# Kernel optimization log

Hardware: AMD Instinct MI355X
Metric: run time of the kernel (lower is better)

The kernel has to match this reference:

```python
import jax, jax.numpy as jnp
import numpy as np

PH, PW, RANK, N_ITER = 7, 7, 8, 5


def _khatri_rao(a, b):
    # a:[I,R], b:[J,R] -> [I*J,R], row index i*J+j (tensorly convention)
    return (a[:, None, :] * b[None, :, :]).reshape(-1, a.shape[1])


def _unfold(t, mode):
    return jnp.moveaxis(t, mode, 0).reshape(t.shape[mode], -1)


def cp_als(t, rank, n_iter, key):
    # CP decomposition via ALS (tensorly parafac, init='random', fixed n_iter,
    # normalize_factors=False -> weights are ones)
    dims = t.shape
    keys = jax.random.split(key, len(dims))
    factors = [jax.random.uniform(keys[i], (dims[i], rank), dtype=t.dtype)
               for i in range(len(dims))]
    unfoldings = [_unfold(t, n) for n in range(len(dims))]
    for _ in range(n_iter):
        for n in range(len(dims)):
            others = [factors[m] for m in range(len(dims)) if m != n]
            kr = _khatri_rao(others[0], others[1])
            mttkrp = unfoldings[n] @ kr
            v = (others[0].T @ others[0]) * (others[1].T @ others[1])
            factors[n] = mttkrp @ jnp.linalg.pinv(v)
    return jnp.ones((rank,), dtype=t.dtype), factors


def setup_inputs() -> dict:
    key = jax.random.key(0)
    k1, _ = jax.random.split(key)
    x = jax.random.normal(k1, (8, 64, 224, 224), dtype=jnp.float32)
    beta = jnp.zeros((1,), dtype=jnp.float32)
    return {"x": x, "beta": beta}


def reference(x, beta):
    B, C, H, W = x.shape
    Hb, Wb = H // PH, W // PW
    M, P = Hb * Wb, PH * PW
    # unfold (kernel == stride, non-overlapping) -> FM:[B*M, P, C]
    FM = x.reshape(B, C, Hb, PH, Wb, PW).transpose(0, 2, 4, 3, 5, 1)
    FM = FM.reshape(B * M, P, C)
    # patch-wise attention scores [B*M, P, P]
    Sc = jax.nn.softmax(jnp.einsum('npc,nqc->npq', FM, FM), axis=-1)
    # patch-wise covariance (mean over channel dim)
    FMc = FM - FM.mean(axis=-1, keepdims=True)
    cov_big = jnp.einsum('npc,nqc->npq', FMc, FMc) / C
    cov_global = cov_big.mean(axis=0, keepdims=True)  # [1, P, P]
    # CP(ALS) decomposition of the global covariance tensor
    weights, (f0, f1, f2) = cp_als(cov_global, RANK, N_ITER, jax.random.key(42))
    w = weights * f0[0]                      # [rank]
    cov_cp = (f1 * w[None, :]) @ f2.T        # [P, P]
    L = Sc + cov_cp[None, :, :]
    Ec = jnp.einsum('npq,nqc->npc', L, FM)   # [B*M, P, C]
    # fold back to [B, C, H, W]
    Ec_map = Ec.reshape(B, Hb, Wb, PH, PW, C).transpose(0, 5, 1, 3, 2, 4)
    Ec_map = Ec_map.reshape(B, C, H, W)
    att_map = beta * Ec_map + x
    out = x * att_map
    return (out, Sc.reshape(B, M, P, P), cov_big.reshape(B, M, P, P), Ec_map)
```

## Files before the change

kernel.cpp:

```cpp
#include <hip/hip_runtime.h>

#define NPATCH   8192
#define PP2      2401
#define CH_STR   50176
#define B_STR    3211264
#define OFF_SC   25690112
#define OFF_COV  45359104
#define OFF_EC   65028096

__device__ __forceinline__ unsigned rotl32(unsigned v, unsigned r){ return (v<<r)|(v>>(32u-r)); }

__device__ __forceinline__ void threefry2x32(unsigned k0, unsigned k1,
                                             unsigned x0, unsigned x1,
                                             unsigned &o0, unsigned &o1){
  unsigned ks2 = k0 ^ k1 ^ 0x1BD11BDAu;
  x0 += k0; x1 += k1;
#define TFR(r) x0 += x1; x1 = rotl32(x1,(r)); x1 ^= x0;
  TFR(13) TFR(15) TFR(26) TFR(6)
  x0 += k1;  x1 += ks2 + 1u;
  TFR(17) TFR(29) TFR(16) TFR(24)
  x0 += ks2; x1 += k0 + 2u;
  TFR(13) TFR(15) TFR(26) TFR(6)
  x0 += k0;  x1 += k1 + 3u;
  TFR(17) TFR(29) TFR(16) TFR(24)
  x0 += k1;  x1 += ks2 + 4u;
  TFR(13) TFR(15) TFR(26) TFR(6)
  x0 += ks2; x1 += k0 + 5u;
#undef TFR
  o0 = x0; o1 = x1;
}

__device__ __forceinline__ float u01f(unsigned b){
  return __uint_as_float((b>>9) | 0x3f800000u) - 1.0f;
}

__global__ __launch_bounds__(256) void k_stats(const float* __restrict__ x,
                                               float* __restrict__ sc_out,
                                               float* __restrict__ cov_out){
  __shared__ float fmt[4][64*49];
  __shared__ float mbuf[4][49], mxb[4][49], ivb[4][49];
  const int t = threadIdx.x, w = t>>6, lane = t&63;
  const int n = (blockIdx.x<<2) + w;
  const int b = n>>10, rem = n&1023, hb = rem>>5, wb = rem&31;
  const float* xp = x + b*B_STR + (hb*7)*224 + wb*7;
  float* fm = fmt[w];

  for (int i=0;i<49;i++){
    int idx = lane + (i<<6);
    int c = idx/49; int p = idx - 49*c; int ph = p/7; int pw = p - 7*ph;
    fm[c*49+p] = xp[c*CH_STR + ph*224 + pw];
  }
  __syncthreads();

  if (lane < 49){
    float s = 0.f;
    for (int k=0;k<64;k++) s += fm[k*49+lane];
    mbuf[w][lane] = s * 0.015625f;
  }

  {
    const int ti = lane/7, tj = lane - 7*(lane/7);
    float acc[7][7];
    if (lane < 49){
      #pragma unroll
      for (int r=0;r<7;r++)
        #pragma unroll
        for (int s=0;s<7;s++) acc[r][s] = 0.f;
      for (int k=0;k<64;k++){
        float av[7], bv[7];
        #pragma unroll
        for (int r=0;r<7;r++) av[r] = fm[k*49 + 7*ti + r];
        #pragma unroll
        for (int s=0;s<7;s++) bv[s] = fm[k*49 + 7*tj + s];
        #pragma unroll
        for (int r=0;r<7;r++)
          #pragma unroll
          for (int s=0;s<7;s++) acc[r][s] = fmaf(av[r], bv[s], acc[r][s]);
      }
    }
    __syncthreads();
    if (lane < 49){
      #pragma unroll
      for (int r=0;r<7;r++)
        #pragma unroll
        for (int s=0;s<7;s++) fm[(7*ti+r)*49 + 7*tj + s] = acc[r][s];
    }
  }
  __syncthreads();

  if (lane < 49){
    float mx = -3.0e38f;
    for (int q=0;q<49;q++) mx = fmaxf(mx, fm[lane*49+q]);
    float s = 0.f;
    for (int q=0;q<49;q++) s += __expf(fm[lane*49+q]-mx);
    mxb[w][lane] = mx; ivb[w][lane] = 1.f/s;
  }
  __syncthreads();

  float* scp = sc_out + (long)n*PP2;
  float* cvp = cov_out + (long)n*PP2;
  for (int i=lane;i<PP2;i+=64){
    int p = i/49, q = i - 49*p;
    float g = fm[i];
    scp[i] = __expf(g - mxb[w][p]) * ivb[w][p];
    cvp[i] = g*0.015625f - mbuf[w][p]*mbuf[w][q];
  }
}

__global__ __launch_bounds__(256) void k_reduce(const float* __restrict__ cov,
                                                double* __restrict__ part){
  const int c = blockIdx.x;
  const float* base = cov + (long)c*32*PP2;
  for (int i=threadIdx.x; i<PP2; i+=256){
    double a0=0.0,a1=0.0,a2=0.0,a3=0.0;
    #pragma unroll
    for (int n=0;n<32;n+=4){
      a0 += (double)base[(n+0)*PP2+i];
      a1 += (double)base[(n+1)*PP2+i];
      a2 += (double)base[(n+2)*PP2+i];
      a3 += (double)base[(n+3)*PP2+i];
    }
    part[(long)c*PP2+i] = (a0+a1)+(a2+a3);
  }
}

__device__ __forceinline__ void gj8_inv(double Aval, int t, double* __restrict__ Vinv){
  const int i = t>>3, j = t&7;
  double A = Aval;
  double B = (i==j) ? 1.0 : 0.0;
  #pragma unroll
  for (int k=0;k<8;k++){
    double piv = __shfl(A, k*9, 64);
    double rp  = 1.0 / piv;
    double Akj = __shfl(A, (k<<3)+j, 64);
    double Bkj = __shfl(B, (k<<3)+j, 64);
    double fac = __shfl(A, (i<<3)+k, 64);
    if (i == k){ A *= rp; B *= rp; }
    else { double f = fac*rp; A -= f*Akj; B -= f*Bkj; }
  }
  Vinv[t] = B;
}

__global__ __launch_bounds__(256) void k_als(const double* __restrict__ part,
                                             float* __restrict__ cov_cp){
  __shared__ double Td[PP2];
  __shared__ double f0[8], f1[49*8], f2[49*8], Pb[49*8], tmp[49*8];
  __shared__ double G1[64], G2[64], Vinv[64], Mv[8];
  __shared__ unsigned sw[6];
  const int t = threadIdx.x;

  for (int i=t;i<PP2;i+=256){
    double s = 0.0;
    for (int c=0;c<256;c++) s += part[(long)c*PP2+i];
    Td[i] = s * (1.0/8192.0);
  }

  if (t < 3){ unsigned a,b2; threefry2x32(0u,42u,0u,(unsigned)t,a,b2); sw[2*t]=a; sw[2*t+1]=b2; }
  __syncthreads();
  if (t < 8){ unsigned a,b2; threefry2x32(sw[0],sw[1],0u,(unsigned)t,a,b2);
              f0[t]=(double)u01f(a^b2); }
  for (int i=t;i<392;i+=256){
    unsigned a,b2;
    threefry2x32(sw[2],sw[3],0u,(unsigned)i,a,b2); f1[i]=(double)u01f(a^b2);
    threefry2x32(sw[4],sw[5],0u,(unsigned)i,a,b2); f2[i]=(double)u01f(a^b2);
  }
  __syncthreads();

  for (int it=0; it<5; ++it){
    for (int i=t;i<392;i+=256){
      int p=i>>3, r=i&7; double s=0.0;
      for (int q=0;q<49;q++) s += Td[p*49+q]*f2[(q<<3)+r];
      Pb[i]=s;
    }
    __syncthreads();
    if (t < 64){ int r=t>>3, s2=t&7; double g=0.0;
      for (int p=0;p<49;p++) g += f1[(p<<3)+r]*f1[(p<<3)+s2]; G1[t]=g;
    } else if (t < 128){ int u=t-64, r=u>>3, s2=u&7; double g=0.0;
      for (int q=0;q<49;q++) g += f2[(q<<3)+r]*f2[(q<<3)+s2]; G2[u]=g;
    } else if (t < 136){ int r=t-128; double m=0.0;
      for (int p=0;p<49;p++) m += f1[(p<<3)+r]*Pb[(p<<3)+r]; Mv[r]=m;
    }
    __syncthreads();
    if (t < 64) gj8_inv(G1[t]*G2[t], t, Vinv);
    __syncthreads();
    if (t < 8){ double s=0.0;
      for (int k=0;k<8;k++) s += Mv[k]*Vinv[(k<<3)+t];
      f0[t]=s;
    }
    __syncthreads();
    if (t < 64){ int r=t>>3, s2=t&7; gj8_inv(f0[r]*f0[s2]*G2[t], t, Vinv); }
    __syncthreads();
    for (int i=t;i<392;i+=256){
      int p=i>>3, r=i&7; double s=0.0;
      #pragma unroll
      for (int k=0;k<8;k++) s += Pb[(p<<3)+k]*f0[k]*Vinv[(k<<3)+r];
      tmp[i]=s;
    }
    __syncthreads();
    for (int i=t;i<392;i+=256) f1[i]=tmp[i];
    __syncthreads();
    for (int i=t;i<392;i+=256){
      int q=i>>3, r=i&7; double s=0.0;
      for (int p=0;p<49;p++) s += Td[q*49+p]*f1[(p<<3)+r];
      Pb[i]=s;
    }
    __syncthreads();
    if (t < 64){ int r=t>>3, s2=t&7; double g=0.0;
      for (int p=0;p<49;p++) g += f1[(p<<3)+r]*f1[(p<<3)+s2]; G1[t]=g;
    }
    __syncthreads();
    if (t < 64){ int r=t>>3, s2=t&7; gj8_inv(f0[r]*f0[s2]*G1[t], t, Vinv); }
    __syncthreads();
    for (int i=t;i<392;i+=256){
      int q=i>>3, r=i&7; double s=0.0;
      #pragma unroll
      for (int k=0;k<8;k++) s += Pb[(q<<3)+k]*f0[k]*Vinv[(k<<3)+r];
      tmp[i]=s;
    }
    __syncthreads();
    for (int i=t;i<392;i+=256) f2[i]=tmp[i];
    __syncthreads();
  }

  for (int i=t;i<PP2;i+=256){
    int p=i/49, q=i-49*(i/49);
    double s=0.0;
    #pragma unroll
    for (int r=0;r<8;r++) s += f1[(p<<3)+r]*f0[r]*f2[(q<<3)+r];
    cov_cp[i] = (float)s;
  }
}

__global__ __launch_bounds__(192) void k_apply(const float* __restrict__ x,
                                               const float* __restrict__ beta_p,
                                               const float* __restrict__ cov_cp,
                                               float* __restrict__ out0,
                                               float* __restrict__ ec_out){
  __shared__ float fmt[3][64*49];
  __shared__ float gbuf[3][PP2];
  __shared__ float mxb[3][49], ivb[3][49];
  const int t = threadIdx.x, w = t>>6, lane = t&63;
  const int n = blockIdx.x*3 + w;
  const bool act = (n < NPATCH);
  const float beta = beta_p[0];
  int b=0, hb=0, wb=0;
  if (act){ b = n>>10; int rem = n&1023; hb = rem>>5; wb = rem&31; }
  const int pbase = b*B_STR + (hb*7)*224 + wb*7;
  float* fm = fmt[w];
  float* G  = gbuf[w];

  if (act){
    for (int i=0;i<49;i++){
      int idx = lane + (i<<6);
      int c = idx/49; int p = idx - 49*c; int ph = p/7; int pw = p - 7*ph;
      fm[c*49+p] = x[pbase + c*CH_STR + ph*224 + pw];
    }
  }
  __syncthreads();

  {
    const int ti = lane/7, tj = lane - 7*(lane/7);
    if (act && lane < 49){
      float acc[7][7];
      #pragma unroll
      for (int r=0;r<7;r++)
        #pragma unroll
        for (int s=0;s<7;s++) acc[r][s] = 0.f;
      for (int k=0;k<64;k++){
        float av[7], bv[7];
        #pragma unroll
        for (int r=0;r<7;r++) av[r] = fm[k*49 + 7*ti + r];
        #pragma unroll
        for (int s=0;s<7;s++) bv[s] = fm[k*49 + 7*tj + s];
        #pragma unroll
        for (int r=0;r<7;r++)
          #pragma unroll
          for (int s=0;s<7;s++) acc[r][s] = fmaf(av[r], bv[s], acc[r][s]);
      }
      #pragma unroll
      for (int r=0;r<7;r++)
        #pragma unroll
        for (int s=0;s<7;s++) G[(7*ti+r)*49 + 7*tj + s] = acc[r][s];
    }
  }
  __syncthreads();

  if (act && lane < 49){
    float mx = -3.0e38f;
    for (int q=0;q<49;q++) mx = fmaxf(mx, G[lane*49+q]);
    float s = 0.f;
    for (int q=0;q<49;q++) s += __expf(G[lane*49+q]-mx);
    mxb[w][lane] = mx; ivb[w][lane] = 1.f/s;
  }
  __syncthreads();

  if (act){
    for (int i=lane;i<PP2;i+=64){
      int p = i/49;
      G[i] = __expf(G[i]-mxb[w][p])*ivb[w][p] + cov_cp[i];
    }
  }
  __syncthreads();

  float a2[7][8];
  const int ti2 = lane>>3, cj = lane&7;
  if (act && lane < 56){
    #pragma unroll
    for (int r=0;r<7;r++)
      #pragma unroll
      for (int s=0;s<8;s++) a2[r][s] = 0.f;
    for (int q=0;q<49;q++){
      float lr[7], fv[8];
      #pragma unroll
      for (int r=0;r<7;r++) lr[r] = G[(7*ti2+r)*49 + q];
      #pragma unroll
      for (int s=0;s<8;s++) fv[s] = fm[((cj<<3)+s)*49 + q];
      #pragma unroll
      for (int r=0;r<7;r++)
        #pragma unroll
        for (int s=0;s<8;s++) a2[r][s] = fmaf(lr[r], fv[s], a2[r][s]);
    }
  }
  __syncthreads();
  if (act && lane < 56){
    #pragma unroll
    for (int r=0;r<7;r++)
      #pragma unroll
      for (int s=0;s<8;s++) fm[((cj<<3)+s)*49 + 7*ti2 + r] = a2[r][s];
  }
  __syncthreads();
  if (act){
    for (int i=lane;i<3136;i+=64){
      int c = i/49; int p = i - 49*c; int ph = p/7; int pw = p - 7*ph;
      int adr = pbase + c*CH_STR + ph*224 + pw;
      float ec = fm[i];
      float xv = x[adr];
      ec_out[adr] = ec;
      out0[adr]  = xv * fmaf(beta, ec, xv);
    }
  }
}

extern "C" void kernel_launch(void* const* d_in, const int* in_sizes, int n_in,
                              void* d_out, int out_size, void* d_ws, size_t ws_size,
                              hipStream_t stream){
  (void)in_sizes; (void)n_in; (void)out_size; (void)ws_size;
  const float* x    = (const float*)d_in[0];
  const float* beta = (const float*)d_in[1];
  float* out = (float*)d_out;
  float* sc  = out + OFF_SC;
  float* cov = out + OFF_COV;
  float* ec  = out + OFF_EC;
  double* part  = (double*)ec;
  float* cov_cp = (float*)d_ws;

  k_stats <<<2048, 256, 0, stream>>>(x, sc, cov);
  k_reduce<<<256,  256, 0, stream>>>(cov, part);
  k_als   <<<1,    256, 0, stream>>>(part, cov_cp);
  k_apply <<<2731, 192, 0, stream>>>(x, beta, cov_cp, out, ec);
}
```

Before: 871.9 us.

## Reuse stored softmax in apply, split final reduction, use one-wave blocks

The apply kernel now reads the softmax scores already written by the stats kernel instead of recomputing the 49x49 Gram matrix and softmax. The second-stage covariance reduction moves out of the single-block ALS kernel into a separate 10-block kernel. Both per-patch kernels switch to 64-thread single-wave blocks, and apply keeps the x values in registers for the epilogue instead of reloading them from global memory. The cost is reading about 80MB of Sc back from memory in place of compute, one extra launch, and higher register pressure from the 49-element register array.

```diff
diff --git a/kernel.cpp b/kernel.cpp
--- a/kernel.cpp
+++ b/kernel.cpp
@@ -34,16 +34,15 @@
   return __uint_as_float((b>>9) | 0x3f800000u) - 1.0f;
 }
 
-__global__ __launch_bounds__(256) void k_stats(const float* __restrict__ x,
-                                               float* __restrict__ sc_out,
-                                               float* __restrict__ cov_out){
-  __shared__ float fmt[4][64*49];
-  __shared__ float mbuf[4][49], mxb[4][49], ivb[4][49];
-  const int t = threadIdx.x, w = t>>6, lane = t&63;
-  const int n = (blockIdx.x<<2) + w;
+__global__ __launch_bounds__(64) void k_stats(const float* __restrict__ x,
+                                              float* __restrict__ sc_out,
+                                              float* __restrict__ cov_out){
+  __shared__ float fm[64*49];
+  __shared__ float mbuf[49], mxb[49], ivb[49];
+  const int lane = threadIdx.x;
+  const int n = blockIdx.x;
   const int b = n>>10, rem = n&1023, hb = rem>>5, wb = rem&31;
   const float* xp = x + b*B_STR + (hb*7)*224 + wb*7;
-  float* fm = fmt[w];
 
   for (int i=0;i<49;i++){
     int idx = lane + (i<<6);
@@ -55,7 +54,7 @@
   if (lane < 49){
     float s = 0.f;
     for (int k=0;k<64;k++) s += fm[k*49+lane];
-    mbuf[w][lane] = s * 0.015625f;
+    mbuf[lane] = s * 0.015625f;
   }
 
   {
@@ -93,7 +92,7 @@
     for (int q=0;q<49;q++) mx = fmaxf(mx, fm[lane*49+q]);
     float s = 0.f;
     for (int q=0;q<49;q++) s += __expf(fm[lane*49+q]-mx);
-    mxb[w][lane] = mx; ivb[w][lane] = 1.f/s;
+    mxb[lane] = mx; ivb[lane] = 1.f/s;
   }
   __syncthreads();
 
@@ -102,8 +101,8 @@
   for (int i=lane;i<PP2;i+=64){
     int p = i/49, q = i - 49*p;
     float g = fm[i];
-    scp[i] = __expf(g - mxb[w][p]) * ivb[w][p];
-    cvp[i] = g*0.015625f - mbuf[w][p]*mbuf[w][q];
+    scp[i] = __expf(g - mxb[p]) * ivb[p];
+    cvp[i] = g*0.015625f - mbuf[p]*mbuf[q];
   }
 }
 
@@ -121,6 +120,16 @@
       a3 += (double)base[(n+3)*PP2+i];
     }
     part[(long)c*PP2+i] = (a0+a1)+(a2+a3);
+  }
+}
+
+__global__ __launch_bounds__(256) void k_reduce2(const double* __restrict__ part,
+                                                 double* __restrict__ td){
+  const int i = blockIdx.x*256 + threadIdx.x;
+  if (i < PP2){
+    double s = 0.0;
+    for (int c=0;c<256;c++) s += part[(long)c*PP2+i];
+    td[i] = s * (1.0/8192.0);
   }
 }
 
@@ -141,7 +150,7 @@
   Vinv[t] = B;
 }
 
-__global__ __launch_bounds__(256) void k_als(const double* __restrict__ part,
+__global__ __launch_bounds__(256) void k_als(const double* __restrict__ td_g,
                                              float* __restrict__ cov_cp){
   __shared__ double Td[PP2];
   __shared__ double f0[8], f1[49*8], f2[49*8], Pb[49*8], tmp[49*8];
@@ -149,11 +158,7 @@
   __shared__ unsigned sw[6];
   const int t = threadIdx.x;
 
-  for (int i=t;i<PP2;i+=256){
-    double s = 0.0;
-    for (int c=0;c<256;c++) s += part[(long)c*PP2+i];
-    Td[i] = s * (1.0/8192.0);
-  }
+  for (int i=t;i<PP2;i+=256) Td[i] = td_g[i];
 
   if (t < 3){ unsigned a,b2; threefry2x32(0u,42u,0u,(unsigned)t,a,b2); sw[2*t]=a; sw[2*t+1]=b2; }
   __syncthreads();
@@ -231,80 +236,36 @@
   }
 }
 
-__global__ __launch_bounds__(192) void k_apply(const float* __restrict__ x,
-                                               const float* __restrict__ beta_p,
-                                               const float* __restrict__ cov_cp,
-                                               float* __restrict__ out0,
-                                               float* __restrict__ ec_out){
-  __shared__ float fmt[3][64*49];
-  __shared__ float gbuf[3][PP2];
-  __shared__ float mxb[3][49], ivb[3][49];
-  const int t = threadIdx.x, w = t>>6, lane = t&63;
-  const int n = blockIdx.x*3 + w;
-  const bool act = (n < NPATCH);
+__global__ __launch_bounds__(64) void k_apply(const float* __restrict__ x,
+                                              const float* __restrict__ beta_p,
+                                              const float* __restrict__ cov_cp,
+                                              const float* __restrict__ sc_in,
+                                              float* __restrict__ out0,
+                                              float* __restrict__ ec_out){
+  __shared__ float fm[64*49];
+  __shared__ float G[PP2];
+  const int lane = threadIdx.x;
+  const int n = blockIdx.x;
   const float beta = beta_p[0];
-  int b=0, hb=0, wb=0;
-  if (act){ b = n>>10; int rem = n&1023; hb = rem>>5; wb = rem&31; }
+  const int b = n>>10, rem = n&1023, hb = rem>>5, wb = rem&31;
   const int pbase = b*B_STR + (hb*7)*224 + wb*7;
-  float* fm = fmt[w];
-  float* G  = gbuf[w];
-
-  if (act){
-    for (int i=0;i<49;i++){
-      int idx = lane + (i<<6);
-      int c = idx/49; int p = idx - 49*c; int ph = p/7; int pw = p - 7*ph;
-      fm[c*49+p] = x[pbase + c*CH_STR + ph*224 + pw];
-    }
-  }
-  __syncthreads();
-
-  {
-    const int ti = lane/7, tj = lane - 7*(lane/7);
-    if (act && lane < 49){
-      float acc[7][7];
-      #pragma unroll
-      for (int r=0;r<7;r++)
-        #pragma unroll
-        for (int s=0;s<7;s++) acc[r][s] = 0.f;
-      for (int k=0;k<64;k++){
-        float av[7], bv[7];
-        #pragma unroll
-        for (int r=0;r<7;r++) av[r] = fm[k*49 + 7*ti + r];
-        #pragma unroll
-        for (int s=0;s<7;s++) bv[s] = fm[k*49 + 7*tj + s];
-        #pragma unroll
-        for (int r=0;r<7;r++)
-          #pragma unroll
-          for (int s=0;s<7;s++) acc[r][s] = fmaf(av[r], bv[s], acc[r][s]);
-      }
-      #pragma unroll
-      for (int r=0;r<7;r++)
-        #pragma unroll
-        for (int s=0;s<7;s++) G[(7*ti+r)*49 + 7*tj + s] = acc[r][s];
-    }
-  }
-  __syncthreads();
-
-  if (act && lane < 49){
-    float mx = -3.0e38f;
-    for (int q=0;q<49;q++) mx = fmaxf(mx, G[lane*49+q]);
-    float s = 0.f;
-    for (int q=0;q<49;q++) s += __expf(G[lane*49+q]-mx);
-    mxb[w][lane] = mx; ivb[w][lane] = 1.f/s;
-  }
-  __syncthreads();
-
-  if (act){
-    for (int i=lane;i<PP2;i+=64){
-      int p = i/49;
-      G[i] = __expf(G[i]-mxb[w][p])*ivb[w][p] + cov_cp[i];
-    }
-  }
-  __syncthreads();
+  const float* scp = sc_in + (long)n*PP2;
+
+  for (int i=0;i<49;i++){
+    int idx = lane + (i<<6);
+    int c = idx/49; int p = idx - 49*c; int ph = p/7; int pw = p - 7*ph;
+    fm[c*49+p] = x[pbase + c*CH_STR + ph*224 + pw];
+  }
+  for (int i=lane;i<PP2;i+=64) G[i] = scp[i] + cov_cp[i];
+  __syncthreads();
+
+  float xsave[49];
+  #pragma unroll
+  for (int j=0;j<49;j++) xsave[j] = fm[lane + (j<<6)];
 
   float a2[7][8];
   const int ti2 = lane>>3, cj = lane&7;
-  if (act && lane < 56){
+  if (lane < 56){
     #pragma unroll
     for (int r=0;r<7;r++)
       #pragma unroll
@@ -322,22 +283,22 @@
     }
   }
   __syncthreads();
-  if (act && lane < 56){
+  if (lane < 56){
     #pragma unroll
     for (int r=0;r<7;r++)
       #pragma unroll
       for (int s=0;s<8;s++) fm[((cj<<3)+s)*49 + 7*ti2 + r] = a2[r][s];
   }
   __syncthreads();
-  if (act){
-    for (int i=lane;i<3136;i+=64){
-      int c = i/49; int p = i - 49*c; int ph = p/7; int pw = p - 7*ph;
-      int adr = pbase + c*CH_STR + ph*224 + pw;
-      float ec = fm[i];
-      float xv = x[adr];
-      ec_out[adr] = ec;
-      out0[adr]  = xv * fmaf(beta, ec, xv);
-    }
+  #pragma unroll
+  for (int j=0;j<49;j++){
+    int i = lane + (j<<6);
+    int c = i/49; int p = i - 49*c; int ph = p/7; int pw = p - 7*ph;
+    int adr = pbase + c*CH_STR + ph*224 + pw;
+    float ec = fm[i];
+    float xv = xsave[j];
+    ec_out[adr] = ec;
+    out0[adr]  = xv * fmaf(beta, ec, xv);
   }
 }
 
@@ -352,10 +313,12 @@
   float* cov = out + OFF_COV;
   float* ec  = out + OFF_EC;
   double* part  = (double*)ec;
-  float* cov_cp = (float*)d_ws;
-
-  k_stats <<<2048, 256, 0, stream>>>(x, sc, cov);
-  k_reduce<<<256,  256, 0, stream>>>(cov, part);
-  k_als   <<<1,    256, 0, stream>>>(part, cov_cp);
-  k_apply <<<2731, 192, 0, stream>>>(x, beta, cov_cp, out, ec);
-}
+  double* td    = (double*)d_ws;
+  float* cov_cp = (float*)(td + 2432);
+
+  k_stats  <<<8192, 64,  0, stream>>>(x, sc, cov);
+  k_reduce <<<256,  256, 0, stream>>>(cov, part);
+  k_reduce2<<<10,   256, 0, stream>>>(part, td);
+  k_als    <<<1,    256, 0, stream>>>(td, cov_cp);
+  k_apply  <<<8192, 64,  0, stream>>>(x, beta, cov_cp, sc, out, ec);
+}
```

After: 789.9 us. 1.1x faster.
